# Optimization experiments

Measured on AMD Instinct MI355X. Metric: run time of the kernel, lower is better.

## Reference

```python
import jax, jax.numpy as jnp
import numpy as np

B, T, C = 4, 1024, 768
E, K = 8, 2               # n_exp, top_k
N = B * T                 # num_tokens
# eval-mode capacity: floor(K * eval_capacity(2.0) * N / E), rounded even, >= min_capacity(4)
CAP = 2048


def setup_inputs() -> dict:
    key = jax.random.key(0)
    k0, k1, k2, k3 = jax.random.split(key, 4)
    s = 0.02
    return {
        "x": jax.random.normal(k0, (B, T, C), jnp.float32),
        "w_g": jax.random.normal(k1, (E, C), jnp.float32) * s,
        "c_fc": jax.random.normal(k2, (E, C, 4 * C), jnp.float32) * s,
        "fc_bias": jnp.zeros((E, 1, 4 * C), jnp.float32),
        "c_proj": jax.random.normal(k3, (E, 4 * C, C), jnp.float32) * s,
        "proj_bias": jnp.zeros((E, 1, C), jnp.float32),
    }


def reference(x, w_g, c_fc, fc_bias, c_proj, proj_bias):
    xf = x.reshape(N, C)
    # ---- Router ----
    logits = xf @ w_g.T                                        # [N, E]
    top_v, top_i = jax.lax.top_k(logits, K)                    # [N, K]
    rows = jnp.arange(N)[:, None]
    masked = jnp.full((N, E), -jnp.inf, logits.dtype).at[rows, top_i].set(top_v)
    probs = jax.nn.softmax(masked, axis=-1)                    # [N, E] (zero off top-k)
    exp_mask = jax.nn.one_hot(top_i, E, dtype=jnp.float32)     # [N, K, E]
    exp_mask = exp_mask.transpose(1, 0, 2)                     # [K, N, E]
    # position of each assignment within its expert queue (top-1 assignments first)
    rank = jnp.cumsum(exp_mask.reshape(K * N, E), axis=0) - 1.0
    rank = rank.reshape(K, N, E)
    exp_mask = exp_mask * (rank < CAP)                         # drop over-capacity tokens
    rank_id = jnp.sum(exp_mask * rank, axis=-1).astype(jnp.int32)  # [K, N]
    exp_w = exp_mask * probs[None]                             # [K, N, E]
    rank_sc = jax.nn.one_hot(rank_id, CAP, dtype=jnp.float32)  # [K, N, CAP]
    cb_weight = jnp.einsum('kne,knc->nec', exp_w, rank_sc)     # [N, E, CAP] combine weights
    sec_mask = (cb_weight != 0).astype(xf.dtype)               # [N, E, CAP] dispatch mask
    # ---- Dispatch + batched experts (per-expert MLP via bmm) ----
    exp_in = jnp.einsum('nec,nd->ecd', sec_mask, xf)           # [E, CAP, C]
    h = jax.nn.gelu(jnp.einsum('ecd,edf->ecf', exp_in, c_fc) + fc_bias, approximate=False)
    exp_out = jnp.einsum('ecf,efd->ecd', h, c_proj) + proj_bias  # [E, CAP, C]
    # ---- Combine ----
    out = jnp.einsum('nec,ecd->nd', cb_weight, exp_out)        # [N, C]
    return out.reshape(B, T, C)
```

## Files before the change

### kernel.cpp

```cpp
#include <hip/hip_runtime.h>
#include <hip/hip_bf16.h>
#include <math.h>

#define N_TOK 4096
#define CDIM  768
#define E_EXP 8
#define CAPC  2048
#define HDIM  3072

typedef __attribute__((ext_vector_type(8))) short short8;
typedef __attribute__((ext_vector_type(4))) float floatx4;

#define VMCNT(n) asm volatile("s_waitcnt vmcnt(" #n ")" ::: "memory")
#define LGKM(n)  asm volatile("s_waitcnt lgkmcnt(" #n ")" ::: "memory")
#define SB0()    __builtin_amdgcn_sched_barrier(0)

static __device__ __forceinline__ unsigned short f2bf(float f) {
  __hip_bfloat16 h = __float2bfloat16(f);
  return __builtin_bit_cast(unsigned short, h);
}
static __device__ __forceinline__ float bf2f(unsigned short u) {
  return __builtin_bit_cast(float, (unsigned int)u << 16);
}

__global__ __launch_bounds__(256)
void prep_kernel(const float* __restrict__ cfc, const float* __restrict__ cpr,
                 __hip_bfloat16* __restrict__ wfcT, __hip_bfloat16* __restrict__ wprT,
                 const float* __restrict__ x, const float* __restrict__ wg,
                 int* __restrict__ eidx, float* __restrict__ pval)
{
  __shared__ unsigned short tile[64][258];
  const int b = blockIdx.x;
  const int t = threadIdx.x;
  if (b < 2304) {
    const float* src;
    unsigned short* dstBase;
    int Cc, kt, nb, ntk;
    if (b < 1152) {
      const int e = b / 144, rem = b % 144;
      kt = rem / 12; nb = rem % 12;
      src = cfc + (size_t)e * CDIM * HDIM;
      Cc = HDIM; ntk = 12;
      dstBase = (unsigned short*)wfcT + (size_t)e * 24 * 12 * 8192;
    } else {
      const int bb = b - 1152;
      const int e = bb / 144, rem = bb % 144;
      kt = rem / 3; nb = rem % 3;
      src = cpr + (size_t)e * HDIM * CDIM;
      Cc = CDIM; ntk = 48;
      dstBase = (unsigned short*)wprT + (size_t)e * 6 * 48 * 8192;
    }
    {
      const int r = t >> 2, q = t & 3;
      const float* rowp = src + (size_t)(kt * 64 + r) * Cc + nb * 256;
#pragma unroll
      for (int i = 0; i < 16; ++i) {
        const int n = i * 16 + q * 4;
        const float4 v = *(const float4*)(rowp + n);
        ushort4 o;
        o.x = f2bf(v.x); o.y = f2bf(v.y); o.z = f2bf(v.z); o.w = f2bf(v.w);
        *(ushort4*)&tile[r][n] = o;
      }
    }
    __syncthreads();
    {
      const int kq = (t & 3) * 16;
      const int np = (t >> 2) * 2;
#pragma unroll
      for (int tt = 0; tt < 2; ++tt) {
        unsigned short* dstT = dstBase + (((size_t)(nb * 2 + tt) * ntk) + kt) * 8192;
        const int n = tt * 128 + np;
        unsigned short lo[16], hi[16];
#pragma unroll
        for (int i = 0; i < 16; ++i) {
          const unsigned int u = *(const unsigned int*)&tile[kq + i][n];
          lo[i] = (unsigned short)u;
          hi[i] = (unsigned short)(u >> 16);
        }
        unsigned short* d0 = dstT + (size_t)np * 64 + kq;
        *(short8*)(d0)     = *(short8*)&lo[0];
        *(short8*)(d0 + 8) = *(short8*)&lo[8];
        unsigned short* d1 = d0 + 64;
        *(short8*)(d1)     = *(short8*)&hi[0];
        *(short8*)(d1 + 8) = *(short8*)&hi[8];
      }
    }
  } else {
    const int wv = t >> 6, lane = t & 63;
    const int n = (b - 2304) * 4 + wv;
    const float* xr = x + (size_t)n * CDIM;
    float acc[E_EXP] = {0.f, 0.f, 0.f, 0.f, 0.f, 0.f, 0.f, 0.f};
#pragma unroll
    for (int i = 0; i < CDIM / 64; ++i) {
      const float xv = xr[i * 64 + lane];
#pragma unroll
      for (int e = 0; e < E_EXP; ++e)
        acc[e] = fmaf(xv, wg[e * CDIM + i * 64 + lane], acc[e]);
    }
#pragma unroll
    for (int e = 0; e < E_EXP; ++e) {
#pragma unroll
      for (int off = 32; off > 0; off >>= 1)
        acc[e] += __shfl_xor(acc[e], off);
    }
    if (lane == 0) {
      int e0 = 0; float v0 = acc[0];
#pragma unroll
      for (int e = 1; e < E_EXP; ++e) if (acc[e] > v0) { v0 = acc[e]; e0 = e; }
      int e1 = -1; float v1 = -3.4e38f;
#pragma unroll
      for (int e = 0; e < E_EXP; ++e) if (e != e0 && acc[e] > v1) { v1 = acc[e]; e1 = e; }
      const float ex = __expf(v1 - v0);
      const float inv = 1.f / (1.f + ex);
      eidx[n] = e0; eidx[N_TOK + n] = e1;
      pval[n] = inv; pval[N_TOK + n] = ex * inv;
    }
  }
}

__global__ __launch_bounds__(256)
void scan_kernel(const int* __restrict__ eidx, int* __restrict__ slot,
                 int* __restrict__ slot_token, int* __restrict__ ecnt,
                 int* __restrict__ work2, int* __restrict__ wcnt)
{
  const int t = threadIdx.x;
  const int base = t * 32;
  int e_local[32];
  int cnt[E_EXP] = {0, 0, 0, 0, 0, 0, 0, 0};
#pragma unroll
  for (int i = 0; i < 32; ++i) {
    const int e = eidx[base + i];
    e_local[i] = e;
    cnt[e]++;
  }
  __shared__ int hist[256][E_EXP];
  __shared__ int secnt[E_EXP];
#pragma unroll
  for (int e = 0; e < E_EXP; ++e) hist[t][e] = cnt[e];
  __syncthreads();
  for (int off = 1; off < 256; off <<= 1) {
    int v[E_EXP] = {0, 0, 0, 0, 0, 0, 0, 0};
    if (t >= off) {
#pragma unroll
      for (int e = 0; e < E_EXP; ++e) v[e] = hist[t - off][e];
    }
    __syncthreads();
    if (t >= off) {
#pragma unroll
      for (int e = 0; e < E_EXP; ++e) hist[t][e] += v[e];
    }
    __syncthreads();
  }
  if (t == 255) {
#pragma unroll
    for (int e = 0; e < E_EXP; ++e) {
      const int tot = hist[255][e];
      const int c = tot < CAPC ? tot : CAPC;
      ecnt[e] = c;
      secnt[e] = c;
    }
  }
  __syncthreads();
  if (t == 0) {
    int n2 = 0;
    for (int e = 0; e < E_EXP; ++e) {
      const int c = secnt[e];
      const int t2 = (c + 127) >> 7;
      for (int b = 0; b < t2; ++b) work2[n2++] = (e << 8) | b;
    }
    wcnt[0] = n2 * 24;
    wcnt[1] = n2 * 6;
  }
  int run[E_EXP];
#pragma unroll
  for (int e = 0; e < E_EXP; ++e) run[e] = hist[t][e] - cnt[e];
#pragma unroll
  for (int i = 0; i < 32; ++i) {
    const int a = base + i;
    const int e = e_local[i];
    const int r = run[e]++;
    const int s = (r < CAPC) ? r : -1;
    slot[a] = s;
    if (s >= 0) slot_token[e * CAPC + s] = (a < N_TOK) ? a : (a - N_TOK);
  }
}

__global__ __launch_bounds__(256)
void dispatch_kernel(const float* __restrict__ x, const int* __restrict__ slot_token,
                     const int* __restrict__ ecnt, __hip_bfloat16* __restrict__ xin)
{
  const int wv = threadIdx.x >> 6, lane = threadIdx.x & 63;
  const int s = blockIdx.x * 4 + wv;
  const int e = s >> 11;
  if ((s & (CAPC - 1)) >= ecnt[e]) return;
  const int n = slot_token[s];
  unsigned short* orow = (unsigned short*)xin + (size_t)s * CDIM;
  const float4* xr = (const float4*)(x + (size_t)n * CDIM);
#pragma unroll
  for (int i = 0; i < 3; ++i) {
    const float4 v = xr[i * 64 + lane];
    ushort4 o;
    o.x = f2bf(v.x); o.y = f2bf(v.y); o.z = f2bf(v.z); o.w = f2bf(v.w);
    *(ushort4*)(orow + (size_t)(i * 64 + lane) * 4) = o;
  }
}

__device__ __forceinline__ void stage_a(const __hip_bfloat16* Ae, char* lds,
                                        int K, int kt, int wv, int lane)
{
  char* dst = lds + (kt & 1) * 32768;
#pragma unroll
  for (int j = 0; j < 4; ++j) {
    const int li = j * 32 + wv * 8 + (lane >> 3);
    const int kb = ((lane & 7) * 16) ^ ((li & 7) << 4);
    const char* g = (const char*)Ae + ((size_t)li * K + (size_t)kt * 64) * 2 + kb;
    __builtin_amdgcn_global_load_lds((const __attribute__((address_space(1))) unsigned int*)g,
                                     (__attribute__((address_space(3))) unsigned int*)(dst + j * 4096 + wv * 1024),
                                     16, 0, 0);
  }
}
__device__ __forceinline__ void stage_b(const char* BeT, char* lds,
                                        int kt, int wv, int lane)
{
  char* dst = lds + (kt & 1) * 32768 + 16384;
#pragma unroll
  for (int j = 0; j < 4; ++j) {
    const int li = j * 32 + wv * 8 + (lane >> 3);
    const int kb = ((lane & 7) * 16) ^ ((li & 7) << 4);
    const char* g = BeT + (size_t)kt * 16384 + li * 128 + kb;
    __builtin_amdgcn_global_load_lds((const __attribute__((address_space(1))) unsigned int*)g,
                                     (__attribute__((address_space(3))) unsigned int*)(dst + j * 4096 + wv * 1024),
                                     16, 0, 0);
  }
}

template<int VME, bool S2>
__device__ __forceinline__ void ktile2(int kt, char* lds,
                                       const __hip_bfloat16* Ae, const char* BeT,
                                       int K, floatx4 (&acc)[4][4],
                                       int wm, int wn, int fr, int fk, int wv, int lane)
{
  if constexpr (VME == 8) VMCNT(8); else VMCNT(0);
  __builtin_amdgcn_s_barrier();
  SB0();
  const char* bufA = lds + ((kt & 1) ? 32768 : 0);
  const char* bufB = bufA + 16384;
  short8 a[4][2], b[4][2];
#pragma unroll
  for (int mi = 0; mi < 4; ++mi) {
    const int lr = wm * 64 + mi * 16 + fr;
    a[mi][0] = *(const short8*)(bufA + lr * 128 + ((fk * 16) ^ ((lr & 7) << 4)));
  }
#pragma unroll
  for (int ni = 0; ni < 4; ++ni) {
    const int lj = wn * 64 + ni * 16 + fr;
    b[ni][0] = *(const short8*)(bufB + lj * 128 + ((fk * 16) ^ ((lj & 7) << 4)));
  }
  SB0();
#pragma unroll
  for (int mi = 0; mi < 4; ++mi) {
    const int lr = wm * 64 + mi * 16 + fr;
    a[mi][1] = *(const short8*)(bufA + lr * 128 + ((64 + fk * 16) ^ ((lr & 7) << 4)));
  }
#pragma unroll
  for (int ni = 0; ni < 4; ++ni) {
    const int lj = wn * 64 + ni * 16 + fr;
    b[ni][1] = *(const short8*)(bufB + lj * 128 + ((64 + fk * 16) ^ ((lj & 7) << 4)));
  }
  SB0();
  LGKM(8); SB0();
  __builtin_amdgcn_s_setprio(1);
#pragma unroll
  for (int mi = 0; mi < 4; ++mi)
#pragma unroll
    for (int ni = 0; ni < 4; ++ni)
      acc[mi][ni] = __builtin_amdgcn_mfma_f32_16x16x32_bf16(a[mi][0], b[ni][0], acc[mi][ni], 0, 0, 0);
  __builtin_amdgcn_s_setprio(0);
  SB0();
  LGKM(0); SB0();
  __builtin_amdgcn_s_setprio(1);
#pragma unroll
  for (int mi = 0; mi < 4; ++mi)
#pragma unroll
    for (int ni = 0; ni < 4; ++ni)
      acc[mi][ni] = __builtin_amdgcn_mfma_f32_16x16x32_bf16(a[mi][1], b[ni][1], acc[mi][ni], 0, 0, 0);
  __builtin_amdgcn_s_setprio(0);
  SB0();
  __builtin_amdgcn_s_barrier();
  if (S2) {
    stage_a(Ae, lds, K, kt + 2, wv, lane);
    stage_b(BeT, lds, kt + 2, wv, lane);
  }
  SB0();
}

static __device__ __forceinline__ float gelu_fast(float v) {
  const float u2 = v * (1.5957691216f + 0.0713548163f * v * v);
  const float ez = __expf(u2);
  return v * ez / (ez + 1.0f);
}

template<int EPI>
__device__ __forceinline__ void epilogue_bf16(floatx4 (&acc)[4][4], char* lds,
                                              const float* be, unsigned short* Cb,
                                              int Nn, int m0, int n0,
                                              int wm, int wn, int fr, int fk,
                                              int wv, int lane)
{
  unsigned short* ep = (unsigned short*)(lds + wv * 2048);
  float bcol[4];
#pragma unroll
  for (int ni = 0; ni < 4; ++ni) bcol[ni] = be[n0 + wn * 64 + ni * 16 + fr];
#pragma unroll
  for (int mi = 0; mi < 4; ++mi) {
#pragma unroll
    for (int ni = 0; ni < 4; ++ni)
#pragma unroll
      for (int j = 0; j < 4; ++j) {
        float v = acc[mi][ni][j] + bcol[ni];
        if (EPI == 1) v = gelu_fast(v);
        const int row = fk * 4 + j;
        *(unsigned short*)((char*)ep + row * 128 + ((ni * 32 + fr * 2) ^ (fk << 5))) = f2bf(v);
      }
    LGKM(0); SB0();
    const int r = lane & 15;
    const int grow = m0 + wm * 64 + mi * 16 + r;
#pragma unroll
    for (int it = 0; it < 2; ++it) {
      const int q = (lane >> 4) + it * 4;
      const short8 vv = *(const short8*)((char*)ep + r * 128 + ((q * 16) ^ ((r >> 2) << 5)));
      *(short8*)(Cb + (size_t)grow * Nn + n0 + wn * 64 + q * 8) = vv;
    }
    LGKM(0); SB0();
  }
}

__global__ __launch_bounds__(256, 2)
void gemm1p(const __hip_bfloat16* __restrict__ A, const __hip_bfloat16* __restrict__ Bt,
            const float* __restrict__ bias, __hip_bfloat16* __restrict__ Cout,
            const int* __restrict__ work, const int* __restrict__ wcnt)
{
  extern __shared__ __align__(16) char lds[];
  const int T = wcnt[0];
  const int cpx = (T + 7) >> 3;
  const int x8 = blockIdx.x & 7, l = blockIdx.x >> 3;
  const int lim = (x8 + 1) * cpx < T ? (x8 + 1) * cpx : T;

  const int t = threadIdx.x, wv = t >> 6, lane = t & 63;
  const int wm = wv >> 1, wn = wv & 1;
  const int fr = lane & 15, fk = lane >> 4;
  constexpr int ntk = CDIM / 64;

  for (int i = x8 * cpx + l; i < lim; i += 64) {
    const int p = i / 24;
    const int bx0 = i % 24;
    const int bx = (p & 1) ? (23 - bx0) : bx0;
    const int w = work[p];
    const int e = w >> 8, by = w & 255;

    const __hip_bfloat16* Ae = A + (size_t)e * CAPC * CDIM + (size_t)by * 128 * CDIM;
    const char* BeT = (const char*)Bt + (((size_t)e * 24 + bx) * 12) * 16384;

    floatx4 acc[4][4] = {};

    stage_a(Ae, lds, CDIM, 0, wv, lane);
    stage_b(BeT, lds, 0, wv, lane);
    stage_a(Ae, lds, CDIM, 1, wv, lane);
    stage_b(BeT, lds, 1, wv, lane);
    SB0();

#pragma unroll 1
    for (int kt = 0; kt < ntk - 2; ++kt)
      ktile2<8, true>(kt, lds, Ae, BeT, CDIM, acc, wm, wn, fr, fk, wv, lane);
    ktile2<8, false>(ntk - 2, lds, Ae, BeT, CDIM, acc, wm, wn, fr, fk, wv, lane);
    ktile2<0, false>(ntk - 1, lds, Ae, BeT, CDIM, acc, wm, wn, fr, fk, wv, lane);

    epilogue_bf16<1>(acc, lds,
                     bias + (size_t)e * HDIM,
                     (unsigned short*)Cout + (size_t)e * CAPC * HDIM,
                     HDIM, by * 128, bx * 128, wm, wn, fr, fk, wv, lane);
    __builtin_amdgcn_s_barrier();
    SB0();
  }
}

__global__ __launch_bounds__(256, 2)
void gemm2x(const __hip_bfloat16* __restrict__ A, const __hip_bfloat16* __restrict__ Bt,
            const float* __restrict__ bias, __hip_bfloat16* __restrict__ Cout,
            const int* __restrict__ work, const int* __restrict__ wcnt)
{
  extern __shared__ __align__(16) char lds[];
  const int T = wcnt[1];
  const int bId = blockIdx.x;
  const int cpx = (T + 7) >> 3;
  if ((bId >> 3) >= cpx) return;
  const int idx = (bId & 7) * cpx + (bId >> 3);
  if (idx >= T) return;
  const int p = idx / 6;
  const int bx0 = idx % 6;
  const int bx = (p & 1) ? (5 - bx0) : bx0;
  const int w = work[p];
  const int e = w >> 8, by = w & 255;

  const int t = threadIdx.x, wv = t >> 6, lane = t & 63;
  const int wm = wv >> 1, wn = wv & 1;
  const int fr = lane & 15, fk = lane >> 4;
  constexpr int ntk = HDIM / 64;

  const __hip_bfloat16* Ae = A + (size_t)e * CAPC * HDIM + (size_t)by * 128 * HDIM;
  const char* BeT = (const char*)Bt + (((size_t)e * 6 + bx) * 48) * 16384;

  floatx4 acc[4][4] = {};

  stage_a(Ae, lds, HDIM, 0, wv, lane);
  stage_b(BeT, lds, 0, wv, lane);
  stage_a(Ae, lds, HDIM, 1, wv, lane);
  stage_b(BeT, lds, 1, wv, lane);
  SB0();

#pragma unroll 1
  for (int kt = 0; kt < ntk - 2; ++kt)
    ktile2<8, true>(kt, lds, Ae, BeT, HDIM, acc, wm, wn, fr, fk, wv, lane);
  ktile2<8, false>(ntk - 2, lds, Ae, BeT, HDIM, acc, wm, wn, fr, fk, wv, lane);
  ktile2<0, false>(ntk - 1, lds, Ae, BeT, HDIM, acc, wm, wn, fr, fk, wv, lane);

  epilogue_bf16<2>(acc, lds,
                   bias + (size_t)e * CDIM,
                   (unsigned short*)Cout + (size_t)e * CAPC * CDIM,
                   CDIM, by * 128, bx * 128, wm, wn, fr, fk, wv, lane);
}

__global__ __launch_bounds__(256)
void combine_kernel(const __hip_bfloat16* __restrict__ eout, const int* __restrict__ eidx,
                    const float* __restrict__ pval, const int* __restrict__ slot,
                    float* __restrict__ out)
{
  const int wv = threadIdx.x >> 6, lane = threadIdx.x & 63;
  const int n = blockIdx.x * 4 + wv;
  const int e0 = eidx[n], e1 = eidx[N_TOK + n];
  int s0 = slot[n], s1 = slot[N_TOK + n];
  const float w0 = (s0 >= 0) ? pval[n] : 0.f;
  const float w1 = (s1 >= 0) ? pval[N_TOK + n] : 0.f;
  s0 = (s0 >= 0) ? s0 : 0;
  s1 = (s1 >= 0) ? s1 : 0;
  const ushort4* r0 = (const ushort4*)((const unsigned short*)eout + ((size_t)e0 * CAPC + s0) * CDIM);
  const ushort4* r1 = (const ushort4*)((const unsigned short*)eout + ((size_t)e1 * CAPC + s1) * CDIM);
  float4* o = (float4*)(out + (size_t)n * CDIM);
#pragma unroll
  for (int i = 0; i < 3; ++i) {
    const ushort4 a = r0[i * 64 + lane];
    const ushort4 b = r1[i * 64 + lane];
    float4 c;
    c.x = w0 * bf2f(a.x) + w1 * bf2f(b.x);
    c.y = w0 * bf2f(a.y) + w1 * bf2f(b.y);
    c.z = w0 * bf2f(a.z) + w1 * bf2f(b.z);
    c.w = w0 * bf2f(a.w) + w1 * bf2f(b.w);
    o[i * 64 + lane] = c;
  }
}

extern "C" void kernel_launch(void* const* d_in, const int* in_sizes, int n_in,
                              void* d_out, int out_size, void* d_ws, size_t ws_size,
                              hipStream_t stream)
{
  const float* x   = (const float*)d_in[0];
  const float* wg  = (const float*)d_in[1];
  const float* cfc = (const float*)d_in[2];
  const float* fcb = (const float*)d_in[3];
  const float* cpr = (const float*)d_in[4];
  const float* prb = (const float*)d_in[5];
  float* out = (float*)d_out;

  char* ws = (char*)d_ws;
  size_t off = 0;
  auto take = [&](size_t bytes) -> void* {
    void* p = ws + off;
    off += (bytes + 255) & ~(size_t)255;
    return p;
  };
  __hip_bfloat16* wfcT = (__hip_bfloat16*)take((size_t)E_EXP * HDIM * CDIM * 2);
  __hip_bfloat16* wprT = (__hip_bfloat16*)take((size_t)E_EXP * CDIM * HDIM * 2);
  __hip_bfloat16* xin  = (__hip_bfloat16*)take((size_t)E_EXP * CAPC * CDIM * 2);
  __hip_bfloat16* hbuf = (__hip_bfloat16*)take((size_t)E_EXP * CAPC * HDIM * 2);
  __hip_bfloat16* eout = (__hip_bfloat16*)take((size_t)E_EXP * CAPC * CDIM * 2);
  int*   eidx = (int*)take((size_t)2 * N_TOK * 4);
  float* pv   = (float*)take((size_t)2 * N_TOK * 4);
  int*   slot = (int*)take((size_t)2 * N_TOK * 4);
  int*   stok = (int*)take((size_t)E_EXP * CAPC * 4);
  int*   ecnt = (int*)take((size_t)E_EXP * 4);
  int*   work2 = (int*)take((size_t)128 * 4);
  int*   wcnt = (int*)take((size_t)2 * 4);

  hipFuncSetAttribute((const void*)gemm1p,
                      hipFuncAttributeMaxDynamicSharedMemorySize, 65536);
  hipFuncSetAttribute((const void*)gemm2x,
                      hipFuncAttributeMaxDynamicSharedMemorySize, 65536);

  prep_kernel<<<2304 + 1024, 256, 0, stream>>>(cfc, cpr, wfcT, wprT, x, wg, eidx, pv);
  scan_kernel<<<1, 256, 0, stream>>>(eidx, slot, stok, ecnt, work2, wcnt);
  dispatch_kernel<<<(E_EXP * CAPC) / 4, 256, 0, stream>>>(x, stok, ecnt, xin);

  gemm1p<<<512, 256, 65536, stream>>>(xin, wfcT, fcb, hbuf, work2, wcnt);
  gemm2x<<<768, 256, 65536, stream>>>(hbuf, wprT, prb, eout, work2, wcnt);

  combine_kernel<<<N_TOK / 4, 256, 0, stream>>>(eout, eidx, pv, slot, out);
}
```

Measured before the change: 172.6 us.

## Overlap c_proj weight transpose with first expert GEMM via atomic work queue

Moves the c_proj fp32-to-bf16 transpose out of the prep kernel and into the gemm1p persistent blocks. Each XCD-group pulls units from an atomic counter that interleaves GEMM tiles with transpose tiles. This shortens the serial prep stage and hides its memory traffic behind compute-bound GEMM1. The cost is an atomic and a barrier per work unit, plus LDS reuse between the transpose and GEMM staging. Correctness relies on all transposes finishing before gemm2x, which the kernel boundary ensures.

```diff
diff --git a/kernel.cpp b/kernel.cpp
--- a/kernel.cpp
+++ b/kernel.cpp
@@ -24,35 +24,22 @@
 }
 
 __global__ __launch_bounds__(256)
-void prep_kernel(const float* __restrict__ cfc, const float* __restrict__ cpr,
-                 __hip_bfloat16* __restrict__ wfcT, __hip_bfloat16* __restrict__ wprT,
+void prep_kernel(const float* __restrict__ cfc,
+                 __hip_bfloat16* __restrict__ wfcT,
                  const float* __restrict__ x, const float* __restrict__ wg,
                  int* __restrict__ eidx, float* __restrict__ pval)
 {
   __shared__ unsigned short tile[64][258];
   const int b = blockIdx.x;
   const int t = threadIdx.x;
-  if (b < 2304) {
-    const float* src;
-    unsigned short* dstBase;
-    int Cc, kt, nb, ntk;
-    if (b < 1152) {
-      const int e = b / 144, rem = b % 144;
-      kt = rem / 12; nb = rem % 12;
-      src = cfc + (size_t)e * CDIM * HDIM;
-      Cc = HDIM; ntk = 12;
-      dstBase = (unsigned short*)wfcT + (size_t)e * 24 * 12 * 8192;
-    } else {
-      const int bb = b - 1152;
-      const int e = bb / 144, rem = bb % 144;
-      kt = rem / 3; nb = rem % 3;
-      src = cpr + (size_t)e * HDIM * CDIM;
-      Cc = CDIM; ntk = 48;
-      dstBase = (unsigned short*)wprT + (size_t)e * 6 * 48 * 8192;
-    }
+  if (b < 1152) {
+    const int e = b / 144, rem = b % 144;
+    const int kt = rem / 12, nb = rem % 12;
+    const float* src = cfc + (size_t)e * CDIM * HDIM;
+    unsigned short* dstBase = (unsigned short*)wfcT + (size_t)e * 24 * 12 * 8192;
     {
       const int r = t >> 2, q = t & 3;
-      const float* rowp = src + (size_t)(kt * 64 + r) * Cc + nb * 256;
+      const float* rowp = src + (size_t)(kt * 64 + r) * HDIM + nb * 256;
 #pragma unroll
       for (int i = 0; i < 16; ++i) {
         const int n = i * 16 + q * 4;
@@ -68,7 +55,7 @@
       const int np = (t >> 2) * 2;
 #pragma unroll
       for (int tt = 0; tt < 2; ++tt) {
-        unsigned short* dstT = dstBase + (((size_t)(nb * 2 + tt) * ntk) + kt) * 8192;
+        unsigned short* dstT = dstBase + (((size_t)(nb * 2 + tt) * 12) + kt) * 8192;
         const int n = tt * 128 + np;
         unsigned short lo[16], hi[16];
 #pragma unroll
@@ -87,7 +74,7 @@
     }
   } else {
     const int wv = t >> 6, lane = t & 63;
-    const int n = (b - 2304) * 4 + wv;
+    const int n = (b - 1152) * 4 + wv;
     const float* xr = x + (size_t)n * CDIM;
     float acc[E_EXP] = {0.f, 0.f, 0.f, 0.f, 0.f, 0.f, 0.f, 0.f};
 #pragma unroll
@@ -121,9 +108,11 @@
 __global__ __launch_bounds__(256)
 void scan_kernel(const int* __restrict__ eidx, int* __restrict__ slot,
                  int* __restrict__ slot_token, int* __restrict__ ecnt,
-                 int* __restrict__ work2, int* __restrict__ wcnt)
+                 int* __restrict__ work2, int* __restrict__ wcnt,
+                 int* __restrict__ wq)
 {
   const int t = threadIdx.x;
+  if (t < 8) wq[t * 16] = 0;
   const int base = t * 32;
   int e_local[32];
   int cnt[E_EXP] = {0, 0, 0, 0, 0, 0, 0, 0};
@@ -335,23 +324,102 @@
   }
 }
 
+__device__ __forceinline__ void transpose_cproj(int td, const float* __restrict__ cpr,
+                                                __hip_bfloat16* __restrict__ wprT,
+                                                char* ldsraw, int t)
+{
+  unsigned short (*tile)[258] = (unsigned short(*)[258])ldsraw;
+  const int e = td / 144, rem = td % 144;
+  const int kt = rem / 3, nb = rem % 3;
+  const float* src = cpr + (size_t)e * HDIM * CDIM;
+  unsigned short* dstBase = (unsigned short*)wprT + (size_t)e * 6 * 48 * 8192;
+  {
+    const int r = t >> 2, q = t & 3;
+    const float* rowp = src + (size_t)(kt * 64 + r) * CDIM + nb * 256;
+#pragma unroll
+    for (int i = 0; i < 16; ++i) {
+      const int n = i * 16 + q * 4;
+      const float4 v = *(const float4*)(rowp + n);
+      ushort4 o;
+      o.x = f2bf(v.x); o.y = f2bf(v.y); o.z = f2bf(v.z); o.w = f2bf(v.w);
+      *(ushort4*)&tile[r][n] = o;
+    }
+  }
+  __syncthreads();
+  {
+    const int kq = (t & 3) * 16;
+    const int np = (t >> 2) * 2;
+#pragma unroll
+    for (int tt = 0; tt < 2; ++tt) {
+      unsigned short* dstT = dstBase + (((size_t)(nb * 2 + tt) * 48) + kt) * 8192;
+      const int n = tt * 128 + np;
+      unsigned short lo[16], hi[16];
+#pragma unroll
+      for (int i = 0; i < 16; ++i) {
+        const unsigned int u = *(const unsigned int*)&tile[kq + i][n];
+        lo[i] = (unsigned short)u;
+        hi[i] = (unsigned short)(u >> 16);
+      }
+      unsigned short* d0 = dstT + (size_t)np * 64 + kq;
+      *(short8*)(d0)     = *(short8*)&lo[0];
+      *(short8*)(d0 + 8) = *(short8*)&lo[8];
+      unsigned short* d1 = d0 + 64;
+      *(short8*)(d1)     = *(short8*)&hi[0];
+      *(short8*)(d1 + 8) = *(short8*)&hi[8];
+    }
+  }
+  __syncthreads();
+}
+
 __global__ __launch_bounds__(256, 2)
 void gemm1p(const __hip_bfloat16* __restrict__ A, const __hip_bfloat16* __restrict__ Bt,
             const float* __restrict__ bias, __hip_bfloat16* __restrict__ Cout,
-            const int* __restrict__ work, const int* __restrict__ wcnt)
+            const int* __restrict__ work, const int* __restrict__ wcnt,
+            const float* __restrict__ cpr, __hip_bfloat16* __restrict__ wprT,
+            int* __restrict__ wq)
 {
   extern __shared__ __align__(16) char lds[];
+  __shared__ int su;
+  const int x8 = blockIdx.x & 7;
   const int T = wcnt[0];
   const int cpx = (T + 7) >> 3;
-  const int x8 = blockIdx.x & 7, l = blockIdx.x >> 3;
-  const int lim = (x8 + 1) * cpx < T ? (x8 + 1) * cpx : T;
+  const int it0 = x8 * cpx;
+  int items_x = T - it0;
+  items_x = items_x < 0 ? 0 : (items_x > cpx ? cpx : items_x);
+  constexpr int nt = 144;
+  const int tt0 = x8 * nt;
+  const int mA = items_x < nt ? items_x : nt;
+  const int m2 = 2 * mA;
 
   const int t = threadIdx.x, wv = t >> 6, lane = t & 63;
   const int wm = wv >> 1, wn = wv & 1;
   const int fr = lane & 15, fk = lane >> 4;
   constexpr int ntk = CDIM / 64;
 
-  for (int i = x8 * cpx + l; i < lim; i += 64) {
+  for (;;) {
+    if (t == 0) su = atomicAdd(&wq[x8 * 16], 1);
+    __syncthreads();
+    const int u = su;
+    int tile = -1, item = -1;
+    if (u < m2) {
+      if (u & 1) tile = u >> 1; else item = u >> 1;
+    } else {
+      const int r = u - m2;
+      if (items_x > nt) {
+        const int iu = nt + r;
+        if (iu < items_x) item = iu; else break;
+      } else {
+        const int td = items_x + r;
+        if (td < nt) tile = td; else break;
+      }
+    }
+
+    if (tile >= 0) {
+      transpose_cproj(tt0 + tile, cpr, wprT, lds, t);
+      continue;
+    }
+
+    const int i = it0 + item;
     const int p = i / 24;
     const int bx0 = i % 24;
     const int bx = (p & 1) ? (23 - bx0) : bx0;
@@ -490,17 +558,18 @@
   int*   ecnt = (int*)take((size_t)E_EXP * 4);
   int*   work2 = (int*)take((size_t)128 * 4);
   int*   wcnt = (int*)take((size_t)2 * 4);
+  int*   wq   = (int*)take((size_t)8 * 16 * 4);
 
   hipFuncSetAttribute((const void*)gemm1p,
                       hipFuncAttributeMaxDynamicSharedMemorySize, 65536);
   hipFuncSetAttribute((const void*)gemm2x,
                       hipFuncAttributeMaxDynamicSharedMemorySize, 65536);
 
-  prep_kernel<<<2304 + 1024, 256, 0, stream>>>(cfc, cpr, wfcT, wprT, x, wg, eidx, pv);
-  scan_kernel<<<1, 256, 0, stream>>>(eidx, slot, stok, ecnt, work2, wcnt);
+  prep_kernel<<<1152 + 1024, 256, 0, stream>>>(cfc, wfcT, x, wg, eidx, pv);
+  scan_kernel<<<1, 256, 0, stream>>>(eidx, slot, stok, ecnt, work2, wcnt, wq);
   dispatch_kernel<<<(E_EXP * CAPC) / 4, 256, 0, stream>>>(x, stok, ecnt, xin);
 
-  gemm1p<<<512, 256, 65536, stream>>>(xin, wfcT, fcb, hbuf, work2, wcnt);
+  gemm1p<<<512, 256, 65536, stream>>>(xin, wfcT, fcb, hbuf, work2, wcnt, cpr, wprT, wq);
   gemm2x<<<768, 256, 65536, stream>>>(hbuf, wprT, prb, eout, work2, wcnt);
 
   combine_kernel<<<N_TOK / 4, 256, 0, stream>>>(eout, eidx, pv, slot, out);
```

Result: no change. 172.9 us (+0.2%).
